# Kernel optimization log

Hardware: AMD Instinct MI355X
Metric: run time of the kernel (lower is better)

## Reference

```python
import jax, jax.numpy as jnp
import numpy as np

N_E = 4096
E_DIM = 256
BETA = 0.25


def setup_inputs() -> dict:
    key = jax.random.key(0)
    k1, k2 = jax.random.split(key)
    z = jax.random.normal(k1, (2, E_DIM, 8, 32, 32), dtype=jnp.float32)
    # torch: embedding.weight.data.uniform_(-1/n_e, 1/n_e)
    embedding_weight = jax.random.uniform(
        k2, (N_E, E_DIM), dtype=jnp.float32, minval=-1.0 / N_E, maxval=1.0 / N_E)
    ema_embedding = jnp.zeros((N_E, E_DIM), dtype=jnp.float32)
    return {"z": z, "embedding_weight": embedding_weight, "ema_embedding": ema_embedding}


def reference(z, embedding_weight, ema_embedding):
    sg = jax.lax.stop_gradient
    # [B, C, D, H, W] -> [B, D, H, W, C]
    zp = jnp.transpose(z, (0, 2, 3, 4, 1))
    zf = zp.reshape(-1, E_DIM)  # [N, e_dim]
    # pairwise squared distances: ||z||^2 + ||e||^2 - 2 z e^T  -> [N, n_e]
    d = (jnp.sum(zf * zf, axis=1, keepdims=True)
         + jnp.sum(embedding_weight * embedding_weight, axis=1)
         - 2.0 * jnp.matmul(zf, embedding_weight.T))
    min_encoding_indices = jnp.argmin(d, axis=1)  # [N]
    min_encodings = jax.nn.one_hot(min_encoding_indices, N_E, dtype=zf.dtype)  # [N, n_e]
    # one_hot @ W == gather of codebook rows
    z_q = embedding_weight[min_encoding_indices].reshape(zp.shape)
    loss = (jnp.mean((sg(z_q) - zp) ** 2)
            + BETA * jnp.mean((z_q - sg(zp)) ** 2))
    # straight-through estimator
    z_q_st = zp + sg(z_q - zp)
    # EMA buffer update (torch does this under no_grad)
    ema_new = BETA * ema_embedding + (1.0 - BETA) * sg(embedding_weight)
    e_mean = jnp.mean(min_encodings, axis=0)
    perplexity = jnp.exp(-jnp.sum(e_mean * jnp.log(e_mean + 1e-10)))
    z_q_out = jnp.transpose(z_q_st, (0, 4, 1, 2, 3))
    z_out = jnp.transpose(zp, (0, 4, 1, 2, 3))
    return (loss, z_q_out, perplexity, min_encodings,
            min_encoding_indices[:, None], z_out, ema_new)
```

## Files before the change

### kernel.cpp

```cpp
#include <hip/hip_runtime.h>
#include <math.h>


#define N_E    4096
#define EDIM   256
#define SPAT   8192
#define NROWS  16384
#define ZELEMS 4194304
#define NCHUNK 32
#define NLOSSPARTS 16384

#define OFF_LOSS    0
#define OFF_ZQ      1
#define OFF_PERP    4194305
#define OFF_ONEHOT  4194306
#define OFF_IDX     71303170
#define OFF_ZOUT    71319554
#define OFF_EMA     75513858

#define SCR_WH_F   4
#define SCR_WL_F   524292
#define SCR_BI_F   71319556
#define SCR_BDD_F  71843844
#define SCR_ZH_F   72892420

#define MARG 1.5e-4f
#define GAPM 1.5e-4f

#define PB_W0   0
#define PB_Z0   1024
#define PB_N0   1536
#define PB_H0   1664
#define PB_TOT  1668

typedef unsigned short u16;
typedef short short8 __attribute__((ext_vector_type(8)));
typedef float f32x4 __attribute__((ext_vector_type(4)));
typedef const void __attribute__((address_space(1)))* gas1;
typedef void __attribute__((address_space(3)))* las3;
#define GLOAD16(g, l) __builtin_amdgcn_global_load_lds((gas1)(g), (las3)(l), 16, 0, 0)

__device__ __forceinline__ u16 f2bf(float f) {
    unsigned u = __float_as_uint(f);
    return (u16)((u + 0x7fffu + ((u >> 16) & 1u)) >> 16);
}
__device__ __forceinline__ float bf2f(u16 h) {
    return __uint_as_float(((unsigned)h) << 16);
}

__global__ __launch_bounds__(256) void prep_all_kernel(
        const float* __restrict__ W, const float* __restrict__ ema,
        const float* __restrict__ z,
        u16* __restrict__ wh, u16* __restrict__ wl,
        float* __restrict__ se, float* __restrict__ out_ema,
        u16* __restrict__ zh, float* __restrict__ sz,
        int* __restrict__ ghist) {
    __shared__ float t[128][65];
    __shared__ float szp[4][128];
    const int bx  = blockIdx.x;
    const int tid = threadIdx.x;

    if (bx < PB_Z0) {
        const size_t tt = (size_t)bx * 256 + tid;
        const int code = (int)(tt >> 6);
        const int lane = tid & 63;
        const float4 v = *(const float4*)(W + tt * 4);

        u16 h0 = f2bf(v.x), h1 = f2bf(v.y), h2 = f2bf(v.z), h3 = f2bf(v.w);
        u16 l0 = f2bf(v.x - bf2f(h0)), l1 = f2bf(v.y - bf2f(h1));
        u16 l2 = f2bf(v.z - bf2f(h2)), l3 = f2bf(v.w - bf2f(h3));
        uint2 hp, lp;
        hp.x = (unsigned)h0 | ((unsigned)h1 << 16); hp.y = (unsigned)h2 | ((unsigned)h3 << 16);
        lp.x = (unsigned)l0 | ((unsigned)l1 << 16); lp.y = (unsigned)l2 | ((unsigned)l3 << 16);
        *(uint2*)(wh + tt * 4) = hp;
        *(uint2*)(wl + tt * 4) = lp;

        const float4 e4 = *(const float4*)(ema + tt * 4);
        float4 o4;
        o4.x = 0.25f * e4.x + 0.75f * v.x;
        o4.y = 0.25f * e4.y + 0.75f * v.y;
        o4.z = 0.25f * e4.z + 0.75f * v.z;
        o4.w = 0.25f * e4.w + 0.75f * v.w;
        *(float4*)(out_ema + tt * 4) = o4;

        float s = v.x * v.x + v.y * v.y + v.z * v.z + v.w * v.w;
        #pragma unroll
        for (int off = 32; off > 0; off >>= 1) s += __shfl_down(s, off);
        if (lane == 0) se[code] = s;
    } else if (bx < PB_N0) {
        const int sub = bx - PB_Z0;
        const int sp0 = (sub & 127) * 64, c0 = ((sub >> 7) & 1) * 128, b = sub >> 8;
        const int wid = tid >> 6, lane = tid & 63;
        const float* zb = z + (size_t)b * (EDIM * SPAT);
        #pragma unroll
        for (int it = 0; it < 32; ++it) {
            const int cl = wid + 4 * it;
            t[cl][lane] = zb[(size_t)(c0 + cl) * SPAT + sp0 + lane];
        }
        __syncthreads();
        #pragma unroll
        for (int it = 0; it < 16; ++it) {
            const int r = wid + 4 * it;
            const float v0 = t[2 * lane][r], v1 = t[2 * lane + 1][r];
            const u16 h0 = f2bf(v0), h1 = f2bf(v1);
            const size_t row = (size_t)b * SPAT + sp0 + r;
            ((unsigned*)zh)[row * 128 + (c0 >> 1) + lane] = (unsigned)h0 | ((unsigned)h1 << 16);
        }
    } else if (bx < PB_H0) {
        const int r0 = (bx - PB_N0) * 128;
        const int bb = r0 >> 13;
        const int sp0 = r0 & (SPAT - 1);
        const float* zb = z + (size_t)bb * (EDIM * SPAT) + sp0;
        const int lr = tid & 127, kh = tid >> 7;
        #pragma unroll
        for (int h = 0; h < 2; ++h) {
            const int kq = kh * 2 + h;
            float s = 0.f;
            const float* p = zb + lr + (size_t)(kq * 64) * SPAT;
            for (int k = 0; k < 64; ++k) {
                float v = p[(size_t)k * SPAT];
                s += v * v;
            }
            szp[kq][lr] = s;
        }
        __syncthreads();
        if (tid < 128)
            sz[r0 + tid] = ((szp[0][tid] + szp[1][tid]) + szp[2][tid]) + szp[3][tid];
    } else {
        const int base = (bx - PB_H0) * 1024;
        #pragma unroll
        for (int j = 0; j < 4; ++j) ghist[base + j * 256 + tid] = 0;
    }
}

__global__ __launch_bounds__(256, 3) void argmin_kernel(
        const u16* __restrict__ zh,
        const u16* __restrict__ wh, const u16* __restrict__ wl,
        const float* __restrict__ se, const float* __restrict__ sz,
        float* __restrict__ bDD, int* __restrict__ bI,
        float* __restrict__ out_onehot) {
    __shared__ u16 sW[2][128][64];
    __shared__ u16 sZ[2][128][32];
    __shared__ float mD[2][128];
    __shared__ int   mI[2][128];
    __shared__ float mD2[2][128];

    const int tid = threadIdx.x;
    const int wid = tid >> 6, lane = tid & 63;
    const int wm = wid >> 1, wn = wid & 1;
    const int lq = lane >> 4, lr = lane & 15;
    const int chunk = blockIdx.y;
    const int rbase = blockIdx.x * 128;
    const int cbase = chunk * 128;

    const u16* gw[4];
    #pragma unroll
    for (int i = 0; i < 4; ++i) {
        const int o = i * 256 + tid;
        const int row = o >> 3, g = o & 7, u = g ^ (row & 7);
        const int ks = (u & 3) * 8;
        gw[i] = (u < 4 ? wh : wl) + (size_t)(cbase + row) * EDIM + ks;
    }
    const u16* gz[2];
    #pragma unroll
    for (int j = 0; j < 2; ++j) {
        const int o = j * 256 + tid;
        const int row = o >> 2, g = o & 3, u = g ^ ((row >> 1) & 3);
        gz[j] = zh + (size_t)(rbase + row) * EDIM + u * 8;
    }

    char* sWb = (char*)&sW[0][0][0];
    char* sZb = (char*)&sZ[0][0][0];

    int aoff[4][2], boff[4];
    #pragma unroll
    for (int tt = 0; tt < 4; ++tt) {
        const int cl = wn * 64 + tt * 16 + lr;
        const int s0 = lq ^ (cl & 7);
        aoff[tt][0] = cl * 128 + s0 * 16;
        aoff[tt][1] = cl * 128 + (s0 ^ 4) * 16;
        const int rl = wm * 64 + tt * 16 + lr;
        boff[tt] = rl * 64 + (lq ^ ((rl >> 1) & 3)) * 16;
    }

    f32x4 acc[4][4];
    #pragma unroll
    for (int ci = 0; ci < 4; ++ci)
        #pragma unroll
        for (int rj = 0; rj < 4; ++rj) {
            f32x4 zzz = {0.f, 0.f, 0.f, 0.f};
            acc[ci][rj] = zzz;
        }

    #define STAGE(b) do {                                                      \
        _Pragma("unroll")                                                      \
        for (int i = 0; i < 4; ++i) {                                          \
            GLOAD16(gw[i], sWb + (b) * 16384 + (i * 256 + wid * 64) * 16);     \
            gw[i] += 32;                                                       \
        }                                                                      \
        _Pragma("unroll")                                                      \
        for (int j = 0; j < 2; ++j) {                                          \
            GLOAD16(gz[j], sZb + (b) * 8192 + (j * 256 + wid * 64) * 16);      \
            gz[j] += 32;                                                       \
        }                                                                      \
    } while (0)

    STAGE(0);
    __syncthreads();

    for (int k0 = 0; k0 < 8; ++k0) {
        const int cur = k0 & 1;
        if (k0 < 7) STAGE(cur ^ 1);

        const char* wbase = sWb + cur * 16384;
        const char* zbase = sZb + cur * 8192;
        short8 zb[4];
        #pragma unroll
        for (int rj = 0; rj < 4; ++rj)
            zb[rj] = *(const short8*)(zbase + boff[rj]);
        #pragma unroll
        for (int ci = 0; ci < 4; ++ci) {
            const short8 wah = *(const short8*)(wbase + aoff[ci][0]);
            const short8 wal = *(const short8*)(wbase + aoff[ci][1]);
            #pragma unroll
            for (int rj = 0; rj < 4; ++rj) {
                acc[ci][rj] = __builtin_amdgcn_mfma_f32_16x16x32_bf16(wah, zb[rj], acc[ci][rj], 0, 0, 0);
                acc[ci][rj] = __builtin_amdgcn_mfma_f32_16x16x32_bf16(wal, zb[rj], acc[ci][rj], 0, 0, 0);
            }
        }
        __syncthreads();
    }
    #undef STAGE

    f32x4 sev[4];
    #pragma unroll
    for (int ci = 0; ci < 4; ++ci)
        sev[ci] = *(const f32x4*)(se + cbase + wn * 64 + ci * 16 + lq * 4);

    #pragma unroll
    for (int rj = 0; rj < 4; ++rj) {
        const int rloc = wm * 64 + rj * 16 + lr;
        const float szr = sz[rbase + rloc];
        float b1 = 3.4e38f, b2 = 3.4e38f; int bi1 = 0x7fffffff;
        #pragma unroll
        for (int ci = 0; ci < 4; ++ci) {
            #pragma unroll
            for (int r = 0; r < 4; ++r) {
                const float q = (szr + sev[ci][r]) - 2.0f * acc[ci][rj][r];
                const int code = cbase + wn * 64 + ci * 16 + lq * 4 + r;
                if (q < b1 || (q == b1 && code < bi1)) {
                    b2 = b1; b1 = q; bi1 = code;
                } else if (q < b2) {
                    b2 = q;
                }
            }
        }
        #pragma unroll
        for (int mask = 16; mask <= 32; mask <<= 1) {
            const float od1 = __shfl_xor(b1, mask);
            const int   oi1 = __shfl_xor(bi1, mask);
            const float od2 = __shfl_xor(b2, mask);
            const bool ot = (od1 < b1) || (od1 == b1 && oi1 < bi1);
            if (ot) { b2 = fminf(b1, od2); b1 = od1; bi1 = oi1; }
            else    { b2 = fminf(b2, od1); }
        }
        if (lq == 0) {
            mD[wn][rloc]  = b1;
            mI[wn][rloc]  = bi1;
            mD2[wn][rloc] = b2;
        }
    }
    __syncthreads();
    if (tid < 128) {
        const float d0 = mD[0][tid], d1 = mD[1][tid];
        const int   i0 = mI[0][tid], i1 = mI[1][tid];
        const float s0 = mD2[0][tid], s1 = mD2[1][tid];
        float dm, sm; int im;
        if (d1 < d0 || (d1 == d0 && i1 < i0)) { dm = d1; im = i1; sm = fminf(s1, d0); }
        else                                  { dm = d0; im = i0; sm = fminf(s0, d1); }
        const int row = rbase + tid;
        float2 p; p.x = dm; p.y = sm;
        *(float2*)(bDD + (size_t)row * 64 + chunk * 2) = p;
        bI[(size_t)row * 32 + chunk] = im;
    }

    {
        const int slice = blockIdx.x * 32 + blockIdx.y;
        float* oh = out_onehot + (size_t)slice * 16384;
        const float4 z4 = {0.f, 0.f, 0.f, 0.f};
        #pragma unroll
        for (int it = 0; it < 16; ++it)
            *(float4*)(oh + it * 1024 + tid * 4) = z4;
    }
}

__global__ __launch_bounds__(128) void resolve_kernel(
        const float* __restrict__ z, const float* __restrict__ W,
        const float* __restrict__ se, const float* __restrict__ sz,
        const float* __restrict__ bDD, const int* __restrict__ bI,
        int* __restrict__ idx_ws, float* __restrict__ out_idx,
        float* __restrict__ out_onehot) {
    __shared__ float zr[EDIM];
    __shared__ float rd[128];
    __shared__ int   ri[128];
    __shared__ unsigned smask;
    __shared__ int swin, sskip;
    const int row = blockIdx.x;
    const int tid = threadIdx.x;

    if (tid < 64) {
        const int c = tid & 31;
        const float2 dd = *(const float2*)(bDD + (size_t)row * 64 + c * 2);
        const int    i1 = bI[(size_t)row * 32 + c];
        const float d1 = dd.x;
        float b1 = dd.x, b2 = dd.y; int j1 = i1;
        #pragma unroll
        for (int mask = 16; mask > 0; mask >>= 1) {
            const float od1 = __shfl_xor(b1, mask);
            const int   oj1 = __shfl_xor(j1, mask);
            const float od2 = __shfl_xor(b2, mask);
            const bool ot = (od1 < b1) || (od1 == b1 && oj1 < j1);
            if (ot) { b2 = fminf(b1, od2); b1 = od1; j1 = oj1; }
            else    { b2 = fminf(b2, od1); }
        }
        const unsigned long long m = __ballot(d1 <= b1 + MARG);
        if (tid == 0) {
            smask = (unsigned)(m & 0xffffffffu);
            swin  = j1;
            sskip = (b2 - b1 > GAPM) ? 1 : 0;
        }
    }
    __syncthreads();

    if (sskip) {
        if (tid == 0) {
            idx_ws[row]  = swin;
            out_idx[row] = (float)swin;
            out_onehot[(size_t)row * N_E + swin] = 1.0f;
        }
        return;
    }

    {
        const int b = row >> 13, sp = row & (SPAT - 1);
        zr[tid]       = z[(size_t)b * (EDIM * SPAT) + (size_t)tid * SPAT + sp];
        zr[tid + 128] = z[(size_t)b * (EDIM * SPAT) + (size_t)(tid + 128) * SPAT + sp];
    }
    __syncthreads();

    const float szr = sz[row];
    unsigned cmask = smask;
    float best = 3.4e38f; int bi = 0x7fffffff;
    while (cmask) {
        const int cc = __ffs(cmask) - 1;
        cmask &= cmask - 1;
        const int code = cc * 128 + tid;
        const float* wr = W + (size_t)code * EDIM;
        float s = 0.f;
        for (int k = 0; k < EDIM; ++k) s += zr[k] * wr[k];
        const float q = (szr + se[code]) - 2.0f * s;
        if (q < best || (q == best && code < bi)) { best = q; bi = code; }
    }
    rd[tid] = best; ri[tid] = bi;
    __syncthreads();
    for (int off = 64; off > 0; off >>= 1) {
        if (tid < off) {
            const float od = rd[tid + off]; const int oi = ri[tid + off];
            if (od < rd[tid] || (od == rd[tid] && oi < ri[tid])) {
                rd[tid] = od; ri[tid] = oi;
            }
        }
        __syncthreads();
    }
    if (tid == 0) {
        const int ii = ri[0];
        idx_ws[row]  = ii;
        out_idx[row] = (float)ii;
        out_onehot[(size_t)row * N_E + ii] = 1.0f;
    }
}

__global__ __launch_bounds__(1024) void hist_kernel(const int* __restrict__ idx,
                                                    int* __restrict__ ghist) {
    __shared__ int lh[N_E];
    const int tid = threadIdx.x;
    for (int i = tid; i < N_E; i += 1024) lh[i] = 0;
    __syncthreads();
    atomicAdd(&lh[idx[blockIdx.x * 1024 + tid]], 1);
    __syncthreads();
    for (int c = tid; c < N_E; c += 1024) {
        const int v = lh[c];
        if (v) atomicAdd(&ghist[c], v);
    }
}

__global__ __launch_bounds__(256) void outputs_kernel(
        const float* __restrict__ z, const float* __restrict__ W,
        const int* __restrict__ idx,
        float* __restrict__ zq_out, float* __restrict__ z_out,
        double* __restrict__ loss_parts) {
    const int t  = blockIdx.x * 256 + threadIdx.x;
    const float zv = z[t];
    const int sp = t & (SPAT - 1);
    const int c  = (t >> 13) & 255;
    const int b  = t >> 21;
    const int n  = (b << 13) + sp;
    const int id = idx[n];
    const float e    = W[id * EDIM + c];
    const float diff = e - zv;
    zq_out[t] = zv + diff;
    z_out[t]  = zv;

    double ds = (double)(diff * diff);
    #pragma unroll
    for (int off = 32; off > 0; off >>= 1) ds += __shfl_down(ds, off);
    __shared__ double bsum[4];
    const int lane = threadIdx.x & 63, w = threadIdx.x >> 6;
    if (lane == 0) bsum[w] = ds;
    __syncthreads();
    if (threadIdx.x == 0)
        loss_parts[blockIdx.x] = bsum[0] + bsum[1] + bsum[2] + bsum[3];
}

__global__ __launch_bounds__(1024) void final_kernel(
        const int* __restrict__ ghist, const double* __restrict__ loss_parts,
        float* __restrict__ out_loss, float* __restrict__ out_perp) {
    __shared__ float ps[1024];
    __shared__ double ls[1024];
    const int tid = threadIdx.x;

    float s = 0.f;
    for (int c = tid; c < N_E; c += 1024) {
        const float p = (float)ghist[c] * (1.0f / (float)NROWS);
        s += p * logf(p + 1e-10f);
    }
    double l = 0.0;
    for (int c = tid; c < NLOSSPARTS; c += 1024) l += loss_parts[c];
    ps[tid] = s;
    ls[tid] = l;
    __syncthreads();
    for (int off = 512; off > 0; off >>= 1) {
        if (tid < off) {
            ps[tid] += ps[tid + off];
            ls[tid] += ls[tid + off];
        }
        __syncthreads();
    }
    if (tid == 0) {
        *out_perp = expf(-ps[0]);
        const float m = (float)(ls[0] / (double)ZELEMS);
        *out_loss = m + 0.25f * m;
    }
}

extern "C" void kernel_launch(void* const* d_in, const int* in_sizes, int n_in,
                              void* d_out, int out_size, void* d_ws, size_t ws_size,
                              hipStream_t stream) {
    const float* z   = (const float*)d_in[0];
    const float* W   = (const float*)d_in[1];
    const float* ema = (const float*)d_in[2];
    float* out = (float*)d_out;

    float* out_loss   = out + OFF_LOSS;
    float* out_zq     = out + OFF_ZQ;
    float* out_perp   = out + OFF_PERP;
    float* out_onehot = out + OFF_ONEHOT;
    float* out_idx    = out + OFF_IDX;
    float* out_z      = out + OFF_ZOUT;
    float* out_ema    = out + OFF_EMA;

    u16*   wh  = (u16*)(out + SCR_WH_F);
    u16*   wl  = (u16*)(out + SCR_WL_F);
    int*   bI  = (int*)(out + SCR_BI_F);
    float* bDD = out + SCR_BDD_F;
    u16*   zh  = (u16*)(out + SCR_ZH_F);

    char* ws = (char*)d_ws;
    float*  se    = (float*)ws;
    float*  sz    = (float*)(ws + 16384);
    int*    idxb  = (int*)  (ws + 81920);
    double* lossp = (double*)(ws + 147456);
    int*    ghist = (int*)  (ws + 278528);

    prep_all_kernel<<<PB_TOT, 256, 0, stream>>>(W, ema, z, wh, wl, se, out_ema,
                                                zh, sz, ghist);
    argmin_kernel<<<dim3(NROWS / 128, NCHUNK), 256, 0, stream>>>(
        zh, wh, wl, se, sz, bDD, bI, out_onehot);
    resolve_kernel<<<NROWS, 128, 0, stream>>>(z, W, se, sz, bDD, bI,
                                              idxb, out_idx, out_onehot);
    hist_kernel<<<16, 1024, 0, stream>>>(idxb, ghist);
    outputs_kernel<<<ZELEMS / 256, 256, 0, stream>>>(z, W, idxb, out_zq, out_z,
                                                     lossp);
    final_kernel<<<1, 1024, 0, stream>>>(ghist, lossp, out_loss, out_perp);
}
```

Baseline: 550.5 us.

## Drop low-part bf16 codebook split and widen argmin tie margins

Removes the hi/lo bf16 split of the codebook, so the distance GEMM uses only the high bf16 part. This halves the MFMA count and the W tile traffic and LDS footprint in the argmin kernel, and raises the occupancy hint to 4 blocks per CU. The prep kernel no longer writes the low part. To cover the larger rounding error, the near-tie margins used by the resolve pass are widened. The risk is more rows needing exact fp32 re-resolution, or missed near-ties if the wider margin is still too small.

Result: no change. 547.3 us (-0.6%).

```diff
diff --git a/kernel.cpp b/kernel.cpp
--- a/kernel.cpp
+++ b/kernel.cpp
@@ -19,13 +19,12 @@
 #define OFF_EMA     75513858
 
 #define SCR_WH_F   4
-#define SCR_WL_F   524292
 #define SCR_BI_F   71319556
 #define SCR_BDD_F  71843844
 #define SCR_ZH_F   72892420
 
-#define MARG 1.5e-4f
-#define GAPM 1.5e-4f
+#define MARG 2.0e-4f
+#define GAPM 2.0e-4f
 
 #define PB_W0   0
 #define PB_Z0   1024
@@ -51,7 +50,7 @@
 __global__ __launch_bounds__(256) void prep_all_kernel(
         const float* __restrict__ W, const float* __restrict__ ema,
         const float* __restrict__ z,
-        u16* __restrict__ wh, u16* __restrict__ wl,
+        u16* __restrict__ wh,
         float* __restrict__ se, float* __restrict__ out_ema,
         u16* __restrict__ zh, float* __restrict__ sz,
         int* __restrict__ ghist) {
@@ -67,13 +66,9 @@
         const float4 v = *(const float4*)(W + tt * 4);
 
         u16 h0 = f2bf(v.x), h1 = f2bf(v.y), h2 = f2bf(v.z), h3 = f2bf(v.w);
-        u16 l0 = f2bf(v.x - bf2f(h0)), l1 = f2bf(v.y - bf2f(h1));
-        u16 l2 = f2bf(v.z - bf2f(h2)), l3 = f2bf(v.w - bf2f(h3));
-        uint2 hp, lp;
+        uint2 hp;
         hp.x = (unsigned)h0 | ((unsigned)h1 << 16); hp.y = (unsigned)h2 | ((unsigned)h3 << 16);
-        lp.x = (unsigned)l0 | ((unsigned)l1 << 16); lp.y = (unsigned)l2 | ((unsigned)l3 << 16);
         *(uint2*)(wh + tt * 4) = hp;
-        *(uint2*)(wl + tt * 4) = lp;
 
         const float4 e4 = *(const float4*)(ema + tt * 4);
         float4 o4;
@@ -133,13 +128,12 @@
     }
 }
 
-__global__ __launch_bounds__(256, 3) void argmin_kernel(
-        const u16* __restrict__ zh,
-        const u16* __restrict__ wh, const u16* __restrict__ wl,
+__global__ __launch_bounds__(256, 4) void argmin_kernel(
+        const u16* __restrict__ zh, const u16* __restrict__ wh,
         const float* __restrict__ se, const float* __restrict__ sz,
         float* __restrict__ bDD, int* __restrict__ bI,
         float* __restrict__ out_onehot) {
-    __shared__ u16 sW[2][128][64];
+    __shared__ u16 sW[2][128][32];
     __shared__ u16 sZ[2][128][32];
     __shared__ float mD[2][128];
     __shared__ int   mI[2][128];
@@ -153,32 +147,23 @@
     const int rbase = blockIdx.x * 128;
     const int cbase = chunk * 128;
 
-    const u16* gw[4];
-    #pragma unroll
-    for (int i = 0; i < 4; ++i) {
-        const int o = i * 256 + tid;
-        const int row = o >> 3, g = o & 7, u = g ^ (row & 7);
-        const int ks = (u & 3) * 8;
-        gw[i] = (u < 4 ? wh : wl) + (size_t)(cbase + row) * EDIM + ks;
-    }
-    const u16* gz[2];
+    const u16* gw[2]; const u16* gz[2];
     #pragma unroll
     for (int j = 0; j < 2; ++j) {
         const int o = j * 256 + tid;
         const int row = o >> 2, g = o & 3, u = g ^ ((row >> 1) & 3);
+        gw[j] = wh + (size_t)(cbase + row) * EDIM + u * 8;
         gz[j] = zh + (size_t)(rbase + row) * EDIM + u * 8;
     }
 
     char* sWb = (char*)&sW[0][0][0];
     char* sZb = (char*)&sZ[0][0][0];
 
-    int aoff[4][2], boff[4];
+    int aoff[4], boff[4];
     #pragma unroll
     for (int tt = 0; tt < 4; ++tt) {
         const int cl = wn * 64 + tt * 16 + lr;
-        const int s0 = lq ^ (cl & 7);
-        aoff[tt][0] = cl * 128 + s0 * 16;
-        aoff[tt][1] = cl * 128 + (s0 ^ 4) * 16;
+        aoff[tt] = cl * 64 + (lq ^ ((cl >> 1) & 3)) * 16;
         const int rl = wm * 64 + tt * 16 + lr;
         boff[tt] = rl * 64 + (lq ^ ((rl >> 1) & 3)) * 16;
     }
@@ -194,14 +179,10 @@
 
     #define STAGE(b) do {                                                      \
         _Pragma("unroll")                                                      \
-        for (int i = 0; i < 4; ++i) {                                          \
-            GLOAD16(gw[i], sWb + (b) * 16384 + (i * 256 + wid * 64) * 16);     \
-            gw[i] += 32;                                                       \
-        }                                                                      \
-        _Pragma("unroll")                                                      \
         for (int j = 0; j < 2; ++j) {                                          \
+            GLOAD16(gw[j], sWb + (b) * 8192 + (j * 256 + wid * 64) * 16);      \
             GLOAD16(gz[j], sZb + (b) * 8192 + (j * 256 + wid * 64) * 16);      \
-            gz[j] += 32;                                                       \
+            gw[j] += 32; gz[j] += 32;                                          \
         }                                                                      \
     } while (0)
 
@@ -212,7 +193,7 @@
         const int cur = k0 & 1;
         if (k0 < 7) STAGE(cur ^ 1);
 
-        const char* wbase = sWb + cur * 16384;
+        const char* wbase = sWb + cur * 8192;
         const char* zbase = sZb + cur * 8192;
         short8 zb[4];
         #pragma unroll
@@ -220,13 +201,10 @@
             zb[rj] = *(const short8*)(zbase + boff[rj]);
         #pragma unroll
         for (int ci = 0; ci < 4; ++ci) {
-            const short8 wah = *(const short8*)(wbase + aoff[ci][0]);
-            const short8 wal = *(const short8*)(wbase + aoff[ci][1]);
+            const short8 wah = *(const short8*)(wbase + aoff[ci]);
             #pragma unroll
-            for (int rj = 0; rj < 4; ++rj) {
+            for (int rj = 0; rj < 4; ++rj)
                 acc[ci][rj] = __builtin_amdgcn_mfma_f32_16x16x32_bf16(wah, zb[rj], acc[ci][rj], 0, 0, 0);
-                acc[ci][rj] = __builtin_amdgcn_mfma_f32_16x16x32_bf16(wal, zb[rj], acc[ci][rj], 0, 0, 0);
-            }
         }
         __syncthreads();
     }
@@ -470,7 +448,6 @@
     float* out_ema    = out + OFF_EMA;
 
     u16*   wh  = (u16*)(out + SCR_WH_F);
-    u16*   wl  = (u16*)(out + SCR_WL_F);
     int*   bI  = (int*)(out + SCR_BI_F);
     float* bDD = out + SCR_BDD_F;
     u16*   zh  = (u16*)(out + SCR_ZH_F);
@@ -482,10 +459,10 @@
     double* lossp = (double*)(ws + 147456);
     int*    ghist = (int*)  (ws + 278528);
 
-    prep_all_kernel<<<PB_TOT, 256, 0, stream>>>(W, ema, z, wh, wl, se, out_ema,
+    prep_all_kernel<<<PB_TOT, 256, 0, stream>>>(W, ema, z, wh, se, out_ema,
                                                 zh, sz, ghist);
     argmin_kernel<<<dim3(NROWS / 128, NCHUNK), 256, 0, stream>>>(
-        zh, wh, wl, se, sz, bDD, bI, out_onehot);
+        zh, wh, se, sz, bDD, bI, out_onehot);
     resolve_kernel<<<NROWS, 128, 0, stream>>>(z, W, se, sz, bDD, bI,
                                               idxb, out_idx, out_onehot);
     hist_kernel<<<16, 1024, 0, stream>>>(idxb, ghist);
```
